# Kernel tuning notes

Hardware: AMD Instinct MI355X
Metric: run time of the kernel (lower is better)

Reference implementation:

```python
import jax, jax.numpy as jnp
import numpy as np

N_SRC0, N_DST0 = 200000, 50000
N_DST1 = 10000
D_IN, D_HID = 128, 128


def _sage_mean(h, src, dst, n_dst, W_self, b_self, W_neigh, b_neigh, act):
    # gather messages from src nodes, mean-aggregate per dst node
    msg = h[src]                                             # [E, D]
    agg = jax.ops.segment_sum(msg, dst, num_segments=n_dst)  # [n_dst, D]
    deg = jax.ops.segment_sum(jnp.ones(dst.shape, h.dtype), dst, num_segments=n_dst)
    h_neigh = agg / jnp.maximum(deg, 1.0)[:, None]
    # DGL block convention: dst nodes are the first n_dst src nodes
    rst = h[:n_dst] @ W_self + b_self + h_neigh @ W_neigh + b_neigh
    return jax.nn.relu(rst) if act else rst


def setup_inputs() -> dict:
    key = jax.random.key(0)
    ks = jax.random.split(key, 12)
    s = 1.0 / np.sqrt(D_HID)
    return {
        "features": jax.random.normal(ks[0], (N_SRC0, D_IN), jnp.float32),
        "src0": jax.random.randint(ks[1], (800000,), 0, N_SRC0),
        "dst0": jax.random.randint(ks[2], (800000,), 0, N_DST0),
        "src1": jax.random.randint(ks[3], (160000,), 0, N_DST0),
        "dst1": jax.random.randint(ks[4], (160000,), 0, N_DST1),
        "W_init": jax.random.uniform(ks[5], (D_IN, D_HID), jnp.float32, -s, s),
        "b_init": jax.random.uniform(ks[6], (D_HID,), jnp.float32, -s, s),
        "W_self": jax.random.uniform(ks[7], (D_HID, D_HID), jnp.float32, -s, s),
        "b_self": jax.random.uniform(ks[8], (D_HID,), jnp.float32, -s, s),
        "W_neigh": jax.random.uniform(ks[9], (D_HID, D_HID), jnp.float32, -s, s),
        "b_neigh": jax.random.uniform(ks[10], (D_HID,), jnp.float32, -s, s),
    }


def reference(features, src0, dst0, src1, dst1, W_init, b_init, W_self, b_self, W_neigh, b_neigh):
    # fc_init + activation
    h = jax.nn.relu(features @ W_init + b_init)              # [N_SRC0, D_HID]
    # block 0 (act_flag True), dropout p=0.0 is identity
    h = _sage_mean(h, src0, dst0, N_DST0, W_self, b_self, W_neigh, b_neigh, act=True)
    # block 1 (last block: act_flag False)
    h = _sage_mean(h, src1, dst1, N_DST1, W_self, b_self, W_neigh, b_neigh, act=False)
    return jnp.squeeze(h, axis=1) if h.shape[1] == 1 else h  # h.squeeze(1) no-op for D_HID>1
```

## Files before the change

kernel.cpp:

```cpp
#include <hip/hip_runtime.h>
#include <stdint.h>
#include <stddef.h>


#define DIM 128
constexpr int N_SRC0 = 200000;
constexpr int N_DST0 = 50000;
constexpr int N_DST1 = 10000;
constexpr int E0 = 800000;
constexpr int E1 = 160000;
constexpr int MAXDEG = 64;

typedef __attribute__((ext_vector_type(8))) short bf16x8;
typedef __attribute__((ext_vector_type(4))) float f32x4;

__device__ __forceinline__ uint16_t f2bf(float f) {
  union { float f; uint32_t u; } v; v.f = f;
  return (uint16_t)((v.u + 0x7FFFu + ((v.u >> 16) & 1u)) >> 16);
}
__device__ __forceinline__ float bf2f(uint16_t h) {
  union { uint32_t u; float f; } v; v.u = ((uint32_t)h) << 16;
  return v.f;
}

__global__ __launch_bounds__(512) void prep_w_kernel(
    const float* __restrict__ W0, const float* __restrict__ W1,
    const float* __restrict__ W2, uint16_t* __restrict__ Wf,
    int* __restrict__ cnt, int ncnt) {
  int gid = blockIdx.x * 512 + threadIdx.x;
  if (gid < 3 * 16384) {
    int m = gid >> 14, idx = gid & 16383;
    const float* W = m == 0 ? W0 : (m == 1 ? W1 : W2);
    int j = idx & 7, lane = (idx >> 3) & 63, nt = (idx >> 9) & 7, kc = idx >> 12;
    int k = kc * 32 + (lane >> 4) * 8 + j;
    int n = nt * 16 + (lane & 15);
    Wf[gid] = f2bf(W[k * DIM + n]);
  }
  int z = gid - 3 * 16384;
  if (z >= 0 && z < ncnt) cnt[z] = 0;
}

__global__ __launch_bounds__(256) void place_kernel(
    const int* __restrict__ src0, const int* __restrict__ dst0,
    const int* __restrict__ src1, const int* __restrict__ dst1,
    int* __restrict__ cnt0, int* __restrict__ cnt1,
    int* __restrict__ eslot0, int* __restrict__ eslot1) {
  int part = blockIdx.x & 7;
  int bpp  = gridDim.x >> 3;
  int bidx = blockIdx.x >> 3;
  const int4* s04 = (const int4*)src0;
  const int4* d04 = (const int4*)dst0;
  const int4* s14 = (const int4*)src1;
  const int4* d14 = (const int4*)dst1;

  int lo = part * (N_DST0 / 8), hi = lo + (N_DST0 / 8);
  for (int i = bidx * 256 + threadIdx.x; i < E0 / 4; i += bpp * 256) {
    int4 d = d04[i]; int4 s = s04[i];
    if (d.x >= lo && d.x < hi) { int p = atomicAdd(&cnt0[d.x], 1); if (p < MAXDEG) eslot0[(size_t)d.x * MAXDEG + p] = s.x; }
    if (d.y >= lo && d.y < hi) { int p = atomicAdd(&cnt0[d.y], 1); if (p < MAXDEG) eslot0[(size_t)d.y * MAXDEG + p] = s.y; }
    if (d.z >= lo && d.z < hi) { int p = atomicAdd(&cnt0[d.z], 1); if (p < MAXDEG) eslot0[(size_t)d.z * MAXDEG + p] = s.z; }
    if (d.w >= lo && d.w < hi) { int p = atomicAdd(&cnt0[d.w], 1); if (p < MAXDEG) eslot0[(size_t)d.w * MAXDEG + p] = s.w; }
  }
  int lo1 = part * (N_DST1 / 8), hi1 = lo1 + (N_DST1 / 8);
  for (int i = bidx * 256 + threadIdx.x; i < E1 / 4; i += bpp * 256) {
    int4 d = d14[i]; int4 s = s14[i];
    if (d.x >= lo1 && d.x < hi1) { int p = atomicAdd(&cnt1[d.x], 1); if (p < MAXDEG) eslot1[(size_t)d.x * MAXDEG + p] = s.x; }
    if (d.y >= lo1 && d.y < hi1) { int p = atomicAdd(&cnt1[d.y], 1); if (p < MAXDEG) eslot1[(size_t)d.y * MAXDEG + p] = s.y; }
    if (d.z >= lo1 && d.z < hi1) { int p = atomicAdd(&cnt1[d.z], 1); if (p < MAXDEG) eslot1[(size_t)d.z * MAXDEG + p] = s.z; }
    if (d.w >= lo1 && d.w < hi1) { int p = atomicAdd(&cnt1[d.w], 1); if (p < MAXDEG) eslot1[(size_t)d.w * MAXDEG + p] = s.w; }
  }
}

__global__ __launch_bounds__(256) void fc_init_kernel(
    const float* __restrict__ feat, const uint16_t* __restrict__ Wf,
    const float* __restrict__ bias, uint16_t* __restrict__ hout) {
  __shared__ uint16_t wl[16384];
  {
    const uint4* g = (const uint4*)Wf;
    uint4* s = (uint4*)wl;
    for (int i = threadIdx.x; i < 2048; i += 256) s[i] = g[i];
  }
  __syncthreads();

  const int lane = threadIdx.x & 63;
  const int q = lane >> 4, m16 = lane & 15;
  const int s = blockIdx.x * 4 + (threadIdx.x >> 6);
  if (s >= N_SRC0 / 16) return;

  const float* ap = feat + (size_t)(s * 16 + m16) * DIM + q * 8;
  float4 X[8];
#pragma unroll
  for (int kc = 0; kc < 4; kc++) {
    X[2 * kc]     = *(const float4*)(ap + kc * 32);
    X[2 * kc + 1] = *(const float4*)(ap + kc * 32 + 4);
  }

  float bv[8];
#pragma unroll
  for (int nt = 0; nt < 8; nt++) bv[nt] = bias[nt * 16 + m16];

  f32x4 acc[8];
#pragma unroll
  for (int nt = 0; nt < 8; nt++) acc[nt] = (f32x4){0.f, 0.f, 0.f, 0.f};

#pragma unroll
  for (int kc = 0; kc < 4; kc++) {
    float xs[8] = {X[2 * kc].x, X[2 * kc].y, X[2 * kc].z, X[2 * kc].w,
                   X[2 * kc + 1].x, X[2 * kc + 1].y, X[2 * kc + 1].z, X[2 * kc + 1].w};
    bf16x8 a;
#pragma unroll
    for (int j = 0; j < 8; j++) a[j] = (short)f2bf(xs[j]);
#pragma unroll
    for (int nt = 0; nt < 8; nt++) {
      bf16x8 w = *(const bf16x8*)&wl[((kc * 8 + nt) * 64 + lane) * 8];
      acc[nt] = __builtin_amdgcn_mfma_f32_16x16x32_bf16(a, w, acc[nt], 0, 0, 0);
    }
  }

  int m0 = s * 16;
#pragma unroll
  for (int nt = 0; nt < 8; nt++)
#pragma unroll
    for (int r = 0; r < 4; r++) {
      float v = fmaxf(acc[nt][r] + bv[nt], 0.f);
      hout[(size_t)(m0 + q * 4 + r) * DIM + nt * 16 + m16] = f2bf(v);
    }
}

__global__ __launch_bounds__(256) void agg_kernel(
    const int* __restrict__ eslot, const int* __restrict__ deg,
    const uint16_t* __restrict__ hsrc, uint16_t* __restrict__ hout, int n_dst) {
  int d = (blockIdx.x * 256 + threadIdx.x) >> 6;
  int lane = threadIdx.x & 63;
  if (d >= n_dst) return;
  const int* sl = eslot + (size_t)d * MAXDEG;
  int dg = deg[d];
  int dgc = dg < MAXDEG ? dg : MAXDEG;
  float a0 = 0.f, a1 = 0.f;
  int e = 0;
  for (; e + 4 <= dgc; e += 4) {
    int s0 = sl[e], s1 = sl[e + 1], s2 = sl[e + 2], s3 = sl[e + 3];
    uint32_t p0 = *(const uint32_t*)(hsrc + (size_t)s0 * DIM + lane * 2);
    uint32_t p1 = *(const uint32_t*)(hsrc + (size_t)s1 * DIM + lane * 2);
    uint32_t p2 = *(const uint32_t*)(hsrc + (size_t)s2 * DIM + lane * 2);
    uint32_t p3 = *(const uint32_t*)(hsrc + (size_t)s3 * DIM + lane * 2);
    a0 += bf2f((uint16_t)p0) + bf2f((uint16_t)p1) + bf2f((uint16_t)p2) + bf2f((uint16_t)p3);
    a1 += bf2f((uint16_t)(p0 >> 16)) + bf2f((uint16_t)(p1 >> 16)) +
          bf2f((uint16_t)(p2 >> 16)) + bf2f((uint16_t)(p3 >> 16));
  }
  for (; e < dgc; e++) {
    uint32_t p = *(const uint32_t*)(hsrc + (size_t)sl[e] * DIM + lane * 2);
    a0 += bf2f((uint16_t)p);
    a1 += bf2f((uint16_t)(p >> 16));
  }
  float inv = 1.f / fmaxf((float)dg, 1.f);
  uint32_t o = (uint32_t)f2bf(a0 * inv) | ((uint32_t)f2bf(a1 * inv) << 16);
  *(uint32_t*)(hout + (size_t)d * DIM + lane * 2) = o;
}

template <bool ACT, bool OUT_BF16>
__global__ __launch_bounds__(256) void sage_kernel(
    const uint16_t* __restrict__ hself, const uint16_t* __restrict__ hneigh,
    const uint16_t* __restrict__ WfS, const uint16_t* __restrict__ WfN,
    const float* __restrict__ bS, const float* __restrict__ bN,
    void* __restrict__ outp, int n_dst) {
  __shared__ uint16_t wS[16384];
  __shared__ uint16_t wN[16384];
  {
    const uint4* gS = (const uint4*)WfS;
    const uint4* gN = (const uint4*)WfN;
    uint4* sS = (uint4*)wS;
    uint4* sN = (uint4*)wN;
    for (int i = threadIdx.x; i < 2048; i += 256) { sS[i] = gS[i]; sN[i] = gN[i]; }
  }
  __syncthreads();

  const int lane = threadIdx.x & 63;
  const int q = lane >> 4, m16 = lane & 15;
  const int s = blockIdx.x * 4 + (threadIdx.x >> 6);
  if (s >= n_dst / 16) return;

  size_t ro = (size_t)(s * 16 + m16) * DIM + q * 8;
  bf16x8 XS[4], XN[4];
#pragma unroll
  for (int kc = 0; kc < 4; kc++) {
    XS[kc] = *(const bf16x8*)(hself + ro + kc * 32);
    XN[kc] = *(const bf16x8*)(hneigh + ro + kc * 32);
  }

  float bv[8];
#pragma unroll
  for (int nt = 0; nt < 8; nt++)
    bv[nt] = bS[nt * 16 + m16] + bN[nt * 16 + m16];

  f32x4 acc[8];
#pragma unroll
  for (int nt = 0; nt < 8; nt++) acc[nt] = (f32x4){0.f, 0.f, 0.f, 0.f};

#pragma unroll
  for (int kc = 0; kc < 4; kc++) {
#pragma unroll
    for (int nt = 0; nt < 8; nt++) {
      size_t fo = (size_t)((kc * 8 + nt) * 64 + lane) * 8;
      bf16x8 ws = *(const bf16x8*)&wS[fo];
      bf16x8 wn = *(const bf16x8*)&wN[fo];
      acc[nt] = __builtin_amdgcn_mfma_f32_16x16x32_bf16(XS[kc], ws, acc[nt], 0, 0, 0);
      acc[nt] = __builtin_amdgcn_mfma_f32_16x16x32_bf16(XN[kc], wn, acc[nt], 0, 0, 0);
    }
  }

  int m0 = s * 16;
#pragma unroll
  for (int nt = 0; nt < 8; nt++)
#pragma unroll
    for (int r = 0; r < 4; r++) {
      float v = acc[nt][r] + bv[nt];
      if (ACT) v = fmaxf(v, 0.f);
      size_t o = (size_t)(m0 + q * 4 + r) * DIM + nt * 16 + m16;
      if (OUT_BF16) ((uint16_t*)outp)[o] = f2bf(v);
      else          ((float*)outp)[o] = v;
    }
}

extern "C" void kernel_launch(void* const* d_in, const int* in_sizes, int n_in,
                              void* d_out, int out_size, void* d_ws, size_t ws_size,
                              hipStream_t stream) {
  const float* feat   = (const float*)d_in[0];
  const int* src0     = (const int*)d_in[1];
  const int* dst0     = (const int*)d_in[2];
  const int* src1     = (const int*)d_in[3];
  const int* dst1     = (const int*)d_in[4];
  const float* W_init = (const float*)d_in[5];
  const float* b_init = (const float*)d_in[6];
  const float* W_self = (const float*)d_in[7];
  const float* b_self = (const float*)d_in[8];
  const float* W_neigh= (const float*)d_in[9];
  const float* b_neigh= (const float*)d_in[10];

  char* ws = (char*)d_ws;
  uint16_t* h     = (uint16_t*)(ws + 0);
  uint16_t* h1    = (uint16_t*)(ws + 51200000);
  int*      cnt0  = (int*)(ws + 64000000);
  int*      cnt1  = (int*)(ws + 64200000);
  int*      eslot0= (int*)(ws + 64240000);
  int*      eslot1= (int*)(ws + 77040000);
  uint16_t* hn    = (uint16_t*)(ws + 79600000);
  uint16_t* WfI   = (uint16_t*)(ws + 92400000);
  uint16_t* WfS   = WfI + 16384;
  uint16_t* WfN   = WfS + 16384;

  prep_w_kernel<<<214, 512, 0, stream>>>(W_init, W_self, W_neigh, WfI, cnt0, 60000);
  place_kernel<<<1024, 256, 0, stream>>>(src0, dst0, src1, dst1,
                                         cnt0, cnt1, eslot0, eslot1);

  fc_init_kernel<<<3125, 256, 0, stream>>>(feat, WfI, b_init, h);

  agg_kernel<<<12500, 256, 0, stream>>>(eslot0, cnt0, h, hn, N_DST0);
  sage_kernel<true, true><<<782, 256, 0, stream>>>(h, hn, WfS, WfN,
                                                   b_self, b_neigh, h1, N_DST0);

  agg_kernel<<<2500, 256, 0, stream>>>(eslot1, cnt1, h1, hn, N_DST1);
  sage_kernel<false, false><<<157, 256, 0, stream>>>(h1, hn, WfS, WfN,
                                                     b_self, b_neigh, d_out, N_DST1);
}
```

Before: 309.1 us.

## Fuse all stages into one cooperative persistent kernel with grid syncs

Replaces the seven separate kernel launches with a single cooperative persistent kernel that steps through weight prep, edge placement, fc_init, both aggregations and both SAGE GEMMs, separated by grid-wide syncs. Edge placement now runs on one wave per block while the other three waves compute fc_init at the same time. The aim is to remove launch gaps and overlap the atomic placement with the dense GEMM. The cost is a grid capped at 512 blocks with only one wave per block doing placement, extra grid.sync barriers, and less parallelism than the large non-persistent grids used before.

Result: slower. 803.9 us (+160.1%).

```diff
diff --git a/kernel.cpp b/kernel.cpp
--- a/kernel.cpp
+++ b/kernel.cpp
@@ -1,6 +1,9 @@
 #include <hip/hip_runtime.h>
+#include <hip/hip_cooperative_groups.h>
 #include <stdint.h>
 #include <stddef.h>
+
+namespace cg = cooperative_groups;
 
 
 #define DIM 128
@@ -23,70 +26,10 @@
   return v.f;
 }
 
-__global__ __launch_bounds__(512) void prep_w_kernel(
-    const float* __restrict__ W0, const float* __restrict__ W1,
-    const float* __restrict__ W2, uint16_t* __restrict__ Wf,
-    int* __restrict__ cnt, int ncnt) {
-  int gid = blockIdx.x * 512 + threadIdx.x;
-  if (gid < 3 * 16384) {
-    int m = gid >> 14, idx = gid & 16383;
-    const float* W = m == 0 ? W0 : (m == 1 ? W1 : W2);
-    int j = idx & 7, lane = (idx >> 3) & 63, nt = (idx >> 9) & 7, kc = idx >> 12;
-    int k = kc * 32 + (lane >> 4) * 8 + j;
-    int n = nt * 16 + (lane & 15);
-    Wf[gid] = f2bf(W[k * DIM + n]);
-  }
-  int z = gid - 3 * 16384;
-  if (z >= 0 && z < ncnt) cnt[z] = 0;
-}
-
-__global__ __launch_bounds__(256) void place_kernel(
-    const int* __restrict__ src0, const int* __restrict__ dst0,
-    const int* __restrict__ src1, const int* __restrict__ dst1,
-    int* __restrict__ cnt0, int* __restrict__ cnt1,
-    int* __restrict__ eslot0, int* __restrict__ eslot1) {
-  int part = blockIdx.x & 7;
-  int bpp  = gridDim.x >> 3;
-  int bidx = blockIdx.x >> 3;
-  const int4* s04 = (const int4*)src0;
-  const int4* d04 = (const int4*)dst0;
-  const int4* s14 = (const int4*)src1;
-  const int4* d14 = (const int4*)dst1;
-
-  int lo = part * (N_DST0 / 8), hi = lo + (N_DST0 / 8);
-  for (int i = bidx * 256 + threadIdx.x; i < E0 / 4; i += bpp * 256) {
-    int4 d = d04[i]; int4 s = s04[i];
-    if (d.x >= lo && d.x < hi) { int p = atomicAdd(&cnt0[d.x], 1); if (p < MAXDEG) eslot0[(size_t)d.x * MAXDEG + p] = s.x; }
-    if (d.y >= lo && d.y < hi) { int p = atomicAdd(&cnt0[d.y], 1); if (p < MAXDEG) eslot0[(size_t)d.y * MAXDEG + p] = s.y; }
-    if (d.z >= lo && d.z < hi) { int p = atomicAdd(&cnt0[d.z], 1); if (p < MAXDEG) eslot0[(size_t)d.z * MAXDEG + p] = s.z; }
-    if (d.w >= lo && d.w < hi) { int p = atomicAdd(&cnt0[d.w], 1); if (p < MAXDEG) eslot0[(size_t)d.w * MAXDEG + p] = s.w; }
-  }
-  int lo1 = part * (N_DST1 / 8), hi1 = lo1 + (N_DST1 / 8);
-  for (int i = bidx * 256 + threadIdx.x; i < E1 / 4; i += bpp * 256) {
-    int4 d = d14[i]; int4 s = s14[i];
-    if (d.x >= lo1 && d.x < hi1) { int p = atomicAdd(&cnt1[d.x], 1); if (p < MAXDEG) eslot1[(size_t)d.x * MAXDEG + p] = s.x; }
-    if (d.y >= lo1 && d.y < hi1) { int p = atomicAdd(&cnt1[d.y], 1); if (p < MAXDEG) eslot1[(size_t)d.y * MAXDEG + p] = s.y; }
-    if (d.z >= lo1 && d.z < hi1) { int p = atomicAdd(&cnt1[d.z], 1); if (p < MAXDEG) eslot1[(size_t)d.z * MAXDEG + p] = s.z; }
-    if (d.w >= lo1 && d.w < hi1) { int p = atomicAdd(&cnt1[d.w], 1); if (p < MAXDEG) eslot1[(size_t)d.w * MAXDEG + p] = s.w; }
-  }
-}
-
-__global__ __launch_bounds__(256) void fc_init_kernel(
-    const float* __restrict__ feat, const uint16_t* __restrict__ Wf,
-    const float* __restrict__ bias, uint16_t* __restrict__ hout) {
-  __shared__ uint16_t wl[16384];
-  {
-    const uint4* g = (const uint4*)Wf;
-    uint4* s = (uint4*)wl;
-    for (int i = threadIdx.x; i < 2048; i += 256) s[i] = g[i];
-  }
-  __syncthreads();
-
-  const int lane = threadIdx.x & 63;
+__device__ __forceinline__ void fc_strip(int s, const float* feat,
+                                         const uint16_t* wl, const float* bv,
+                                         uint16_t* hout, int lane) {
   const int q = lane >> 4, m16 = lane & 15;
-  const int s = blockIdx.x * 4 + (threadIdx.x >> 6);
-  if (s >= N_SRC0 / 16) return;
-
   const float* ap = feat + (size_t)(s * 16 + m16) * DIM + q * 8;
   float4 X[8];
 #pragma unroll
@@ -94,15 +37,9 @@
     X[2 * kc]     = *(const float4*)(ap + kc * 32);
     X[2 * kc + 1] = *(const float4*)(ap + kc * 32 + 4);
   }
-
-  float bv[8];
-#pragma unroll
-  for (int nt = 0; nt < 8; nt++) bv[nt] = bias[nt * 16 + m16];
-
   f32x4 acc[8];
 #pragma unroll
   for (int nt = 0; nt < 8; nt++) acc[nt] = (f32x4){0.f, 0.f, 0.f, 0.f};
-
 #pragma unroll
   for (int kc = 0; kc < 4; kc++) {
     float xs[8] = {X[2 * kc].x, X[2 * kc].y, X[2 * kc].z, X[2 * kc].w,
@@ -112,11 +49,10 @@
     for (int j = 0; j < 8; j++) a[j] = (short)f2bf(xs[j]);
 #pragma unroll
     for (int nt = 0; nt < 8; nt++) {
-      bf16x8 w = *(const bf16x8*)&wl[((kc * 8 + nt) * 64 + lane) * 8];
-      acc[nt] = __builtin_amdgcn_mfma_f32_16x16x32_bf16(a, w, acc[nt], 0, 0, 0);
-    }
-  }
-
+      bf16x8 wv = *(const bf16x8*)&wl[((kc * 8 + nt) * 64 + lane) * 8];
+      acc[nt] = __builtin_amdgcn_mfma_f32_16x16x32_bf16(a, wv, acc[nt], 0, 0, 0);
+    }
+  }
   int m0 = s * 16;
 #pragma unroll
   for (int nt = 0; nt < 8; nt++)
@@ -127,12 +63,9 @@
     }
 }
 
-__global__ __launch_bounds__(256) void agg_kernel(
-    const int* __restrict__ eslot, const int* __restrict__ deg,
-    const uint16_t* __restrict__ hsrc, uint16_t* __restrict__ hout, int n_dst) {
-  int d = (blockIdx.x * 256 + threadIdx.x) >> 6;
-  int lane = threadIdx.x & 63;
-  if (d >= n_dst) return;
+__device__ __forceinline__ void agg_dst(int d, const int* eslot, const int* deg,
+                                        const uint16_t* hsrc, uint16_t* hout,
+                                        int lane) {
   const int* sl = eslot + (size_t)d * MAXDEG;
   int dg = deg[d];
   int dgc = dg < MAXDEG ? dg : MAXDEG;
@@ -159,27 +92,11 @@
 }
 
 template <bool ACT, bool OUT_BF16>
-__global__ __launch_bounds__(256) void sage_kernel(
-    const uint16_t* __restrict__ hself, const uint16_t* __restrict__ hneigh,
-    const uint16_t* __restrict__ WfS, const uint16_t* __restrict__ WfN,
-    const float* __restrict__ bS, const float* __restrict__ bN,
-    void* __restrict__ outp, int n_dst) {
-  __shared__ uint16_t wS[16384];
-  __shared__ uint16_t wN[16384];
-  {
-    const uint4* gS = (const uint4*)WfS;
-    const uint4* gN = (const uint4*)WfN;
-    uint4* sS = (uint4*)wS;
-    uint4* sN = (uint4*)wN;
-    for (int i = threadIdx.x; i < 2048; i += 256) { sS[i] = gS[i]; sN[i] = gN[i]; }
-  }
-  __syncthreads();
-
-  const int lane = threadIdx.x & 63;
+__device__ __forceinline__ void sage_strip(int s, const uint16_t* hself,
+                                           const uint16_t* hneigh,
+                                           const uint16_t* wS, const uint16_t* wN,
+                                           const float* bv, void* outp, int lane) {
   const int q = lane >> 4, m16 = lane & 15;
-  const int s = blockIdx.x * 4 + (threadIdx.x >> 6);
-  if (s >= n_dst / 16) return;
-
   size_t ro = (size_t)(s * 16 + m16) * DIM + q * 8;
   bf16x8 XS[4], XN[4];
 #pragma unroll
@@ -187,16 +104,9 @@
     XS[kc] = *(const bf16x8*)(hself + ro + kc * 32);
     XN[kc] = *(const bf16x8*)(hneigh + ro + kc * 32);
   }
-
-  float bv[8];
-#pragma unroll
-  for (int nt = 0; nt < 8; nt++)
-    bv[nt] = bS[nt * 16 + m16] + bN[nt * 16 + m16];
-
   f32x4 acc[8];
 #pragma unroll
   for (int nt = 0; nt < 8; nt++) acc[nt] = (f32x4){0.f, 0.f, 0.f, 0.f};
-
 #pragma unroll
   for (int kc = 0; kc < 4; kc++) {
 #pragma unroll
@@ -208,7 +118,6 @@
       acc[nt] = __builtin_amdgcn_mfma_f32_16x16x32_bf16(XN[kc], wn, acc[nt], 0, 0, 0);
     }
   }
-
   int m0 = s * 16;
 #pragma unroll
   for (int nt = 0; nt < 8; nt++)
@@ -220,6 +129,106 @@
       if (OUT_BF16) ((uint16_t*)outp)[o] = f2bf(v);
       else          ((float*)outp)[o] = v;
     }
+}
+
+__global__ void __launch_bounds__(256, 2) mega_kernel(
+    const float* __restrict__ feat,
+    const int* __restrict__ src0, const int* __restrict__ dst0,
+    const int* __restrict__ src1, const int* __restrict__ dst1,
+    const float* __restrict__ W_init, const float* __restrict__ b_init,
+    const float* __restrict__ W_self, const float* __restrict__ b_self,
+    const float* __restrict__ W_neigh, const float* __restrict__ b_neigh,
+    uint16_t* __restrict__ h, uint16_t* __restrict__ h1, uint16_t* __restrict__ hn,
+    int* cnt0, int* cnt1,
+    int* __restrict__ eslot0, int* __restrict__ eslot1,
+    uint16_t* __restrict__ Wf, float* __restrict__ outp) {
+  __shared__ uint16_t wA[16384];
+  __shared__ uint16_t wB[16384];
+  cg::grid_group grid = cg::this_grid();
+
+  const int tid = threadIdx.x;
+  const int w = tid >> 6, lane = tid & 63;
+  const int m16 = lane & 15;
+  const int gw = blockIdx.x * 4 + w;
+  const int nwav = gridDim.x * 4;
+  const int nthr = gridDim.x * 256;
+  const int gid = blockIdx.x * 256 + tid;
+
+  for (int i = gid; i < 3 * 16384; i += nthr) {
+    int m = i >> 14, idx = i & 16383;
+    const float* W = m == 0 ? W_init : (m == 1 ? W_self : W_neigh);
+    int j = idx & 7, ln = (idx >> 3) & 63, nt = (idx >> 9) & 7, kc = idx >> 12;
+    Wf[i] = f2bf(W[(kc * 32 + (ln >> 4) * 8 + j) * DIM + nt * 16 + (ln & 15)]);
+  }
+  for (int z = gid; z < N_DST0; z += nthr) cnt0[z] = 0;
+  for (int z = gid; z < N_DST1; z += nthr) cnt1[z] = 0;
+  grid.sync();
+
+  {
+    const uint4* g = (const uint4*)Wf;
+    uint4* sdst = (uint4*)wA;
+    for (int i = tid; i < 2048; i += 256) sdst[i] = g[i];
+  }
+  __syncthreads();
+  if (w == 0) {
+    int part = blockIdx.x & 7;
+    int bpp  = gridDim.x >> 3;
+    int bidx = blockIdx.x >> 3;
+    const int4* s04 = (const int4*)src0;
+    const int4* d04 = (const int4*)dst0;
+    const int4* s14 = (const int4*)src1;
+    const int4* d14 = (const int4*)dst1;
+    int lo = part * (N_DST0 / 8), hi = lo + (N_DST0 / 8);
+    for (int i = bidx * 64 + lane; i < E0 / 4; i += bpp * 64) {
+      int4 d = d04[i]; int4 s = s04[i];
+      if (d.x >= lo && d.x < hi) { int p = atomicAdd(&cnt0[d.x], 1); if (p < MAXDEG) eslot0[(size_t)d.x * MAXDEG + p] = s.x; }
+      if (d.y >= lo && d.y < hi) { int p = atomicAdd(&cnt0[d.y], 1); if (p < MAXDEG) eslot0[(size_t)d.y * MAXDEG + p] = s.y; }
+      if (d.z >= lo && d.z < hi) { int p = atomicAdd(&cnt0[d.z], 1); if (p < MAXDEG) eslot0[(size_t)d.z * MAXDEG + p] = s.z; }
+      if (d.w >= lo && d.w < hi) { int p = atomicAdd(&cnt0[d.w], 1); if (p < MAXDEG) eslot0[(size_t)d.w * MAXDEG + p] = s.w; }
+    }
+    int lo1 = part * (N_DST1 / 8), hi1 = lo1 + (N_DST1 / 8);
+    for (int i = bidx * 64 + lane; i < E1 / 4; i += bpp * 64) {
+      int4 d = d14[i]; int4 s = s14[i];
+      if (d.x >= lo1 && d.x < hi1) { int p = atomicAdd(&cnt1[d.x], 1); if (p < MAXDEG) eslot1[(size_t)d.x * MAXDEG + p] = s.x; }
+      if (d.y >= lo1 && d.y < hi1) { int p = atomicAdd(&cnt1[d.y], 1); if (p < MAXDEG) eslot1[(size_t)d.y * MAXDEG + p] = s.y; }
+      if (d.z >= lo1 && d.z < hi1) { int p = atomicAdd(&cnt1[d.z], 1); if (p < MAXDEG) eslot1[(size_t)d.z * MAXDEG + p] = s.z; }
+      if (d.w >= lo1 && d.w < hi1) { int p = atomicAdd(&cnt1[d.w], 1); if (p < MAXDEG) eslot1[(size_t)d.w * MAXDEG + p] = s.w; }
+    }
+  } else {
+    float bv[8];
+#pragma unroll
+    for (int nt = 0; nt < 8; nt++) bv[nt] = b_init[nt * 16 + m16];
+    for (int s = blockIdx.x * 3 + (w - 1); s < N_SRC0 / 16; s += gridDim.x * 3)
+      fc_strip(s, feat, wA, bv, h, lane);
+  }
+  grid.sync();
+
+  for (int d = gw; d < N_DST0; d += nwav) agg_dst(d, eslot0, cnt0, h, hn, lane);
+  grid.sync();
+
+  {
+    const uint4* gS = (const uint4*)(Wf + 16384);
+    const uint4* gN = (const uint4*)(Wf + 32768);
+    uint4* sA = (uint4*)wA;
+    uint4* sB = (uint4*)wB;
+    for (int i = tid; i < 2048; i += 256) { sA[i] = gS[i]; sB[i] = gN[i]; }
+  }
+  __syncthreads();
+  {
+    float bv[8];
+#pragma unroll
+    for (int nt = 0; nt < 8; nt++)
+      bv[nt] = b_self[nt * 16 + m16] + b_neigh[nt * 16 + m16];
+    for (int s = gw; s < N_DST0 / 16; s += nwav)
+      sage_strip<true, true>(s, h, hn, wA, wB, bv, h1, lane);
+    grid.sync();
+
+    for (int d = gw; d < N_DST1; d += nwav) agg_dst(d, eslot1, cnt1, h1, hn, lane);
+    grid.sync();
+
+    for (int s = gw; s < N_DST1 / 16; s += nwav)
+      sage_strip<false, false>(s, h1, hn, wA, wB, bv, outp, lane);
+  }
 }
 
 extern "C" void kernel_launch(void* const* d_in, const int* in_sizes, int n_in,
@@ -245,21 +254,23 @@
   int*      eslot0= (int*)(ws + 64240000);
   int*      eslot1= (int*)(ws + 77040000);
   uint16_t* hn    = (uint16_t*)(ws + 79600000);
-  uint16_t* WfI   = (uint16_t*)(ws + 92400000);
-  uint16_t* WfS   = WfI + 16384;
-  uint16_t* WfN   = WfS + 16384;
-
-  prep_w_kernel<<<214, 512, 0, stream>>>(W_init, W_self, W_neigh, WfI, cnt0, 60000);
-  place_kernel<<<1024, 256, 0, stream>>>(src0, dst0, src1, dst1,
-                                         cnt0, cnt1, eslot0, eslot1);
-
-  fc_init_kernel<<<3125, 256, 0, stream>>>(feat, WfI, b_init, h);
-
-  agg_kernel<<<12500, 256, 0, stream>>>(eslot0, cnt0, h, hn, N_DST0);
-  sage_kernel<true, true><<<782, 256, 0, stream>>>(h, hn, WfS, WfN,
-                                                   b_self, b_neigh, h1, N_DST0);
-
-  agg_kernel<<<2500, 256, 0, stream>>>(eslot1, cnt1, h1, hn, N_DST1);
-  sage_kernel<false, false><<<157, 256, 0, stream>>>(h1, hn, WfS, WfN,
-                                                     b_self, b_neigh, d_out, N_DST1);
-}
+  uint16_t* Wf    = (uint16_t*)(ws + 92400000);
+  float*    outp  = (float*)d_out;
+
+  int maxb = 2;
+  hipOccupancyMaxActiveBlocksPerMultiprocessor(&maxb, (const void*)mega_kernel, 256, 0);
+  int grid = maxb * 256;
+  if (grid > 512) grid = 512;
+  grid &= ~7;
+  if (grid < 8) grid = 8;
+
+  void* args[] = {
+    (void*)&feat, (void*)&src0, (void*)&dst0, (void*)&src1, (void*)&dst1,
+    (void*)&W_init, (void*)&b_init, (void*)&W_self, (void*)&b_self,
+    (void*)&W_neigh, (void*)&b_neigh,
+    (void*)&h, (void*)&h1, (void*)&hn, (void*)&cnt0, (void*)&cnt1,
+    (void*)&eslot0, (void*)&eslot1, (void*)&Wf, (void*)&outp,
+  };
+  hipLaunchCooperativeKernel((const void*)mega_kernel, dim3(grid), dim3(256),
+                             args, 0, stream);
+}
```

## Merge edge placement and fc_init into one launch to overlap them

Applied to the files above, without the earlier changes.

Folds the edge-bucketing (place) kernel and the fc_init GEMM kernel into a single launch. The first 256 blocks do the atomic edge placement and the remaining 3125 blocks do the feature transform, so the two independent stages run at the same time and one launch is saved. Placement now uses 256 blocks instead of 1024, so each placement block handles more edges and may become the long tail. The placement branch is also compiled into a kernel that reserves 32KB of LDS, which can limit how many placement blocks fit on a CU.

Measured after the change: 324.7 us. +5.1%, slower.

```diff
diff --git a/kernel.cpp b/kernel.cpp
--- a/kernel.cpp
+++ b/kernel.cpp
@@ -10,6 +10,7 @@
 constexpr int E0 = 800000;
 constexpr int E1 = 160000;
 constexpr int MAXDEG = 64;
+constexpr int PLACE_BLOCKS = 256;
 
 typedef __attribute__((ext_vector_type(8))) short bf16x8;
 typedef __attribute__((ext_vector_type(4))) float f32x4;
@@ -23,7 +24,7 @@
   return v.f;
 }
 
-__global__ __launch_bounds__(512) void prep_w_kernel(
+__global__ __launch_bounds__(512) void setup_kernel(
     const float* __restrict__ W0, const float* __restrict__ W1,
     const float* __restrict__ W2, uint16_t* __restrict__ Wf,
     int* __restrict__ cnt, int ncnt) {
@@ -32,59 +33,57 @@
     int m = gid >> 14, idx = gid & 16383;
     const float* W = m == 0 ? W0 : (m == 1 ? W1 : W2);
     int j = idx & 7, lane = (idx >> 3) & 63, nt = (idx >> 9) & 7, kc = idx >> 12;
-    int k = kc * 32 + (lane >> 4) * 8 + j;
-    int n = nt * 16 + (lane & 15);
-    Wf[gid] = f2bf(W[k * DIM + n]);
+    Wf[gid] = f2bf(W[(kc * 32 + (lane >> 4) * 8 + j) * DIM + nt * 16 + (lane & 15)]);
   }
   int z = gid - 3 * 16384;
   if (z >= 0 && z < ncnt) cnt[z] = 0;
 }
 
-__global__ __launch_bounds__(256) void place_kernel(
+__global__ __launch_bounds__(256) void fcplace_kernel(
+    const float* __restrict__ feat, const uint16_t* __restrict__ Wf,
+    const float* __restrict__ bias, uint16_t* __restrict__ hout,
     const int* __restrict__ src0, const int* __restrict__ dst0,
     const int* __restrict__ src1, const int* __restrict__ dst1,
     int* __restrict__ cnt0, int* __restrict__ cnt1,
     int* __restrict__ eslot0, int* __restrict__ eslot1) {
-  int part = blockIdx.x & 7;
-  int bpp  = gridDim.x >> 3;
-  int bidx = blockIdx.x >> 3;
-  const int4* s04 = (const int4*)src0;
-  const int4* d04 = (const int4*)dst0;
-  const int4* s14 = (const int4*)src1;
-  const int4* d14 = (const int4*)dst1;
-
-  int lo = part * (N_DST0 / 8), hi = lo + (N_DST0 / 8);
-  for (int i = bidx * 256 + threadIdx.x; i < E0 / 4; i += bpp * 256) {
-    int4 d = d04[i]; int4 s = s04[i];
-    if (d.x >= lo && d.x < hi) { int p = atomicAdd(&cnt0[d.x], 1); if (p < MAXDEG) eslot0[(size_t)d.x * MAXDEG + p] = s.x; }
-    if (d.y >= lo && d.y < hi) { int p = atomicAdd(&cnt0[d.y], 1); if (p < MAXDEG) eslot0[(size_t)d.y * MAXDEG + p] = s.y; }
-    if (d.z >= lo && d.z < hi) { int p = atomicAdd(&cnt0[d.z], 1); if (p < MAXDEG) eslot0[(size_t)d.z * MAXDEG + p] = s.z; }
-    if (d.w >= lo && d.w < hi) { int p = atomicAdd(&cnt0[d.w], 1); if (p < MAXDEG) eslot0[(size_t)d.w * MAXDEG + p] = s.w; }
-  }
-  int lo1 = part * (N_DST1 / 8), hi1 = lo1 + (N_DST1 / 8);
-  for (int i = bidx * 256 + threadIdx.x; i < E1 / 4; i += bpp * 256) {
-    int4 d = d14[i]; int4 s = s14[i];
-    if (d.x >= lo1 && d.x < hi1) { int p = atomicAdd(&cnt1[d.x], 1); if (p < MAXDEG) eslot1[(size_t)d.x * MAXDEG + p] = s.x; }
-    if (d.y >= lo1 && d.y < hi1) { int p = atomicAdd(&cnt1[d.y], 1); if (p < MAXDEG) eslot1[(size_t)d.y * MAXDEG + p] = s.y; }
-    if (d.z >= lo1 && d.z < hi1) { int p = atomicAdd(&cnt1[d.z], 1); if (p < MAXDEG) eslot1[(size_t)d.z * MAXDEG + p] = s.z; }
-    if (d.w >= lo1 && d.w < hi1) { int p = atomicAdd(&cnt1[d.w], 1); if (p < MAXDEG) eslot1[(size_t)d.w * MAXDEG + p] = s.w; }
-  }
-}
-
-__global__ __launch_bounds__(256) void fc_init_kernel(
-    const float* __restrict__ feat, const uint16_t* __restrict__ Wf,
-    const float* __restrict__ bias, uint16_t* __restrict__ hout) {
+  if (blockIdx.x < PLACE_BLOCKS) {
+    int part = blockIdx.x & 7;
+    int bpp  = PLACE_BLOCKS >> 3;
+    int bidx = blockIdx.x >> 3;
+    const int4* s04 = (const int4*)src0;
+    const int4* d04 = (const int4*)dst0;
+    const int4* s14 = (const int4*)src1;
+    const int4* d14 = (const int4*)dst1;
+    int lo = part * (N_DST0 / 8), hi = lo + (N_DST0 / 8);
+    for (int i = bidx * 256 + threadIdx.x; i < E0 / 4; i += bpp * 256) {
+      int4 d = d04[i]; int4 s = s04[i];
+      if (d.x >= lo && d.x < hi) { int p = atomicAdd(&cnt0[d.x], 1); if (p < MAXDEG) eslot0[(size_t)d.x * MAXDEG + p] = s.x; }
+      if (d.y >= lo && d.y < hi) { int p = atomicAdd(&cnt0[d.y], 1); if (p < MAXDEG) eslot0[(size_t)d.y * MAXDEG + p] = s.y; }
+      if (d.z >= lo && d.z < hi) { int p = atomicAdd(&cnt0[d.z], 1); if (p < MAXDEG) eslot0[(size_t)d.z * MAXDEG + p] = s.z; }
+      if (d.w >= lo && d.w < hi) { int p = atomicAdd(&cnt0[d.w], 1); if (p < MAXDEG) eslot0[(size_t)d.w * MAXDEG + p] = s.w; }
+    }
+    int lo1 = part * (N_DST1 / 8), hi1 = lo1 + (N_DST1 / 8);
+    for (int i = bidx * 256 + threadIdx.x; i < E1 / 4; i += bpp * 256) {
+      int4 d = d14[i]; int4 s = s14[i];
+      if (d.x >= lo1 && d.x < hi1) { int p = atomicAdd(&cnt1[d.x], 1); if (p < MAXDEG) eslot1[(size_t)d.x * MAXDEG + p] = s.x; }
+      if (d.y >= lo1 && d.y < hi1) { int p = atomicAdd(&cnt1[d.y], 1); if (p < MAXDEG) eslot1[(size_t)d.y * MAXDEG + p] = s.y; }
+      if (d.z >= lo1 && d.z < hi1) { int p = atomicAdd(&cnt1[d.z], 1); if (p < MAXDEG) eslot1[(size_t)d.z * MAXDEG + p] = s.z; }
+      if (d.w >= lo1 && d.w < hi1) { int p = atomicAdd(&cnt1[d.w], 1); if (p < MAXDEG) eslot1[(size_t)d.w * MAXDEG + p] = s.w; }
+    }
+    return;
+  }
+
   __shared__ uint16_t wl[16384];
   {
     const uint4* g = (const uint4*)Wf;
-    uint4* s = (uint4*)wl;
-    for (int i = threadIdx.x; i < 2048; i += 256) s[i] = g[i];
+    uint4* sdst = (uint4*)wl;
+    for (int i = threadIdx.x; i < 2048; i += 256) sdst[i] = g[i];
   }
   __syncthreads();
 
   const int lane = threadIdx.x & 63;
   const int q = lane >> 4, m16 = lane & 15;
-  const int s = blockIdx.x * 4 + (threadIdx.x >> 6);
+  const int s = (blockIdx.x - PLACE_BLOCKS) * 4 + (threadIdx.x >> 6);
   if (s >= N_SRC0 / 16) return;
 
   const float* ap = feat + (size_t)(s * 16 + m16) * DIM + q * 8;
@@ -112,8 +111,8 @@
     for (int j = 0; j < 8; j++) a[j] = (short)f2bf(xs[j]);
 #pragma unroll
     for (int nt = 0; nt < 8; nt++) {
-      bf16x8 w = *(const bf16x8*)&wl[((kc * 8 + nt) * 64 + lane) * 8];
-      acc[nt] = __builtin_amdgcn_mfma_f32_16x16x32_bf16(a, w, acc[nt], 0, 0, 0);
+      bf16x8 wv = *(const bf16x8*)&wl[((kc * 8 + nt) * 64 + lane) * 8];
+      acc[nt] = __builtin_amdgcn_mfma_f32_16x16x32_bf16(a, wv, acc[nt], 0, 0, 0);
     }
   }
 
@@ -249,11 +248,11 @@
   uint16_t* WfS   = WfI + 16384;
   uint16_t* WfN   = WfS + 16384;
 
-  prep_w_kernel<<<214, 512, 0, stream>>>(W_init, W_self, W_neigh, WfI, cnt0, 60000);
-  place_kernel<<<1024, 256, 0, stream>>>(src0, dst0, src1, dst1,
-                                         cnt0, cnt1, eslot0, eslot1);
-
-  fc_init_kernel<<<3125, 256, 0, stream>>>(feat, WfI, b_init, h);
+  setup_kernel<<<214, 512, 0, stream>>>(W_init, W_self, W_neigh, WfI, cnt0, 60000);
+
+  fcplace_kernel<<<PLACE_BLOCKS + 3125, 256, 0, stream>>>(
+      feat, WfI, b_init, h, src0, dst0, src1, dst1,
+      cnt0, cnt1, eslot0, eslot1);
 
   agg_kernel<<<12500, 256, 0, stream>>>(eslot0, cnt0, h, hn, N_DST0);
   sage_kernel<true, true><<<782, 256, 0, stream>>>(h, hn, WfS, WfN,
```
